# Kernel tuning notes

Hardware: AMD Instinct MI355X
Metric: run time of the kernel (lower is better)

## Reference

```python
import jax, jax.numpy as jnp
import numpy as np

N_NODES = 50000
N_EDGES = 800000
NFEAT = 128
NHID = 128


def gcn_conv(x, edge_index, W, b):
    """PyG GCNConv: add self-loops, symmetric deg^-1/2 normalization, scatter-add."""
    n = x.shape[0]
    loop = jnp.arange(n, dtype=edge_index.dtype)
    row = jnp.concatenate([edge_index[0], loop])  # source nodes
    col = jnp.concatenate([edge_index[1], loop])  # target nodes
    ones = jnp.ones(row.shape[0], dtype=x.dtype)
    deg = jax.ops.segment_sum(ones, col, num_segments=n)
    dinv = jnp.where(deg > 0, jax.lax.rsqrt(deg), 0.0).astype(x.dtype)
    norm = dinv[row] * dinv[col]  # [E+N]
    h = x @ W  # [n, out]
    msg = h[row] * norm[:, None]  # gather + scale, [E+N, out]
    out = jax.ops.segment_sum(msg, col, num_segments=n)  # scatter-add
    return out + b


def setup_inputs() -> dict:
    key = jax.random.key(0)
    kx, ke, k1, k2 = jax.random.split(key, 4)
    x = jax.random.normal(kx, (N_NODES, NFEAT), dtype=jnp.float32)
    edge_index = jax.random.randint(ke, (2, N_EDGES), 0, N_NODES, dtype=jnp.int32)
    s1 = 1.0 / np.sqrt(NFEAT)
    s2 = 1.0 / np.sqrt(NHID)
    W1 = jax.random.uniform(k1, (NFEAT, NHID), jnp.float32, -s1, s1)
    b1 = jnp.zeros((NHID,), jnp.float32)
    W2 = jax.random.uniform(k2, (NHID, NHID), jnp.float32, -s2, s2)
    b2 = jnp.zeros((NHID,), jnp.float32)
    return {"x": x, "edge_index": edge_index, "W1": W1, "b1": b1, "W2": W2, "b2": b2}


def reference(x, edge_index, W1, b1, W2, b2):
    # DGI.forward -> encoder z: relu(GCNConv) x2, dropout=0, no layernorm
    h = jax.nn.relu(gcn_conv(x, edge_index, W1, b1))
    z = jax.nn.relu(gcn_conv(h, edge_index, W2, b2))
    return z
```

## Files before the change

### kernel.cpp

```cpp
#include <hip/hip_runtime.h>
#include <hip/hip_fp16.h>


#define NBK 98
#define BSH 9
#define BCAP 10240

typedef _Float16 f16x8 __attribute__((ext_vector_type(8)));
typedef float f32x4 __attribute__((ext_vector_type(4)));

__global__ __launch_bounds__(256) void k_bucket(const int* __restrict__ row,
                                                const int* __restrict__ col,
                                                int* __restrict__ bcur,
                                                unsigned int* __restrict__ arena,
                                                int E) {
  __shared__ int hist[NBK];
  __shared__ int basec[NBK];
  int tid = threadIdx.x;
  if (tid < NBK) hist[tid] = 0;
  __syncthreads();
  int base = blockIdx.x * 2048;
  int cc[8], rr[8], bb[8];
#pragma unroll
  for (int j = 0; j < 8; ++j) {
    int e = base + j * 256 + tid;
    bb[j] = -1;
    if (e < E) {
      cc[j] = col[e];
      rr[j] = row[e];
      bb[j] = cc[j] >> BSH;
      atomicAdd(&hist[bb[j]], 1);
    }
  }
  __syncthreads();
  if (tid < NBK && hist[tid] > 0)
    basec[tid] = atomicAdd(&bcur[tid], hist[tid]);
  __syncthreads();
#pragma unroll
  for (int j = 0; j < 8; ++j) {
    if (bb[j] >= 0) {
      int pos = atomicAdd(&basec[bb[j]], 1);
      if (pos < BCAP)
        arena[(size_t)bb[j] * BCAP + pos] =
            ((unsigned int)rr[j] << BSH) | (unsigned int)(cc[j] & 511);
    }
  }
}

__global__ __launch_bounds__(256) void k_csr(const int* __restrict__ bcur,
                                             const unsigned int* __restrict__ arena,
                                             int* __restrict__ offs,
                                             float* __restrict__ dinv,
                                             int* __restrict__ esrc, int n) {
  __shared__ int hist[512];
  __shared__ int psum[256];
  int b = blockIdx.x, tid = threadIdx.x;
  hist[tid] = 0;
  hist[tid + 256] = 0;
  __syncthreads();
  int m = min(bcur[b], BCAP);
  const unsigned int* a = arena + (size_t)b * BCAP;
  for (int i = tid; i < m; i += 256) atomicAdd(&hist[a[i] & 511], 1);
  __syncthreads();

  psum[tid] = (tid < b && tid < NBK) ? min(bcur[tid], BCAP) : 0;
  __syncthreads();
#pragma unroll
  for (int d = 128; d > 0; d >>= 1) {
    if (tid < d) psum[tid] += psum[tid + d];
    __syncthreads();
  }
  int base = psum[0];
  __syncthreads();

  int a0 = hist[2 * tid], a1 = hist[2 * tid + 1];
  int pair = a0 + a1;
  psum[tid] = pair;
  __syncthreads();
#pragma unroll
  for (int d = 1; d < 256; d <<= 1) {
    int add = (tid >= d) ? psum[tid - d] : 0;
    __syncthreads();
    psum[tid] += add;
    __syncthreads();
  }
  int excl = psum[tid] - pair;
  int o0 = base + excl, o1 = o0 + a0;

  int nb0 = b << BSH;
  int node0 = nb0 + 2 * tid, node1 = node0 + 1;
  if (node0 < n) {
    offs[node0] = o0;
    dinv[node0] = rsqrtf((float)(a0 + 1));
  }
  if (node1 < n) {
    offs[node1] = o1;
    dinv[node1] = rsqrtf((float)(a1 + 1));
  }
  if (b == NBK - 1 && tid == 255) offs[n] = base + psum[255];
  __syncthreads();

  hist[2 * tid] = o0;
  hist[2 * tid + 1] = o1;
  __syncthreads();
  for (int i = tid; i < m; i += 256) {
    unsigned int p = a[i];
    int pos = atomicAdd(&hist[p & 511], 1);
    esrc[pos] = (int)(p >> BSH);
  }
}

__global__ __launch_bounds__(256) void k_prepW(const float* __restrict__ W1,
                                               const float* __restrict__ W2,
                                               __half* __restrict__ Wt1,
                                               __half* __restrict__ Wt2,
                                               int* __restrict__ bcur) {
  int i = blockIdx.x * 256 + threadIdx.x;
  int n = i >> 7, k = i & 127;
  Wt1[i] = (__half)W1[k * 128 + n];
  Wt2[i] = (__half)W2[k * 128 + n];
  if (i < NBK) bcur[i] = 0;
}

__device__ inline uint4 loadA16(const float* A, int grow, int k16, int M) {
  if (grow >= M) return make_uint4(0, 0, 0, 0);
  const float4* p = (const float4*)(A + (size_t)grow * 128 + k16 * 8);
  float4 f0 = p[0], f1 = p[1];
  __half2 h0 = __floats2half2_rn(f0.x, f0.y);
  __half2 h1 = __floats2half2_rn(f0.z, f0.w);
  __half2 h2 = __floats2half2_rn(f1.x, f1.y);
  __half2 h3 = __floats2half2_rn(f1.z, f1.w);
  uint4 u;
  u.x = *(unsigned int*)&h0;
  u.y = *(unsigned int*)&h1;
  u.z = *(unsigned int*)&h2;
  u.w = *(unsigned int*)&h3;
  return u;
}
__device__ inline uint4 loadA16(const __half* A, int grow, int k16, int M) {
  if (grow >= M) return make_uint4(0, 0, 0, 0);
  return *(const uint4*)(A + (size_t)grow * 128 + k16 * 8);
}

template <typename AT>
__global__ __launch_bounds__(256) void k_gemm(const AT* __restrict__ A,
                                              const __half* __restrict__ Wt,
                                              const float* __restrict__ dinv,
                                              __half* __restrict__ C, int M) {
  __shared__ char smem[16384 + 32768];
  char* Al = smem;
  char* Bl = smem + 16384;
  int tid = threadIdx.x;
  int row0 = blockIdx.x * 64;

  const uint4* Wt4 = (const uint4*)Wt;
#pragma unroll
  for (int i = 0; i < 8; ++i) {
    int c = tid + 256 * i;
    int n = c >> 4, k16 = c & 15;
    uint4 v = Wt4[c];
    *(uint4*)(Bl + n * 256 + ((k16 * 16) ^ ((n & 7) << 4))) = v;
  }
#pragma unroll
  for (int i = 0; i < 4; ++i) {
    int c = tid + 256 * i;
    int r = c >> 4, k16 = c & 15;
    uint4 v = loadA16(A, row0 + r, k16, M);
    *(uint4*)(Al + r * 256 + ((k16 * 16) ^ ((r & 7) << 4))) = v;
  }
  __syncthreads();

  int w = tid >> 6, l = tid & 63;
  int lr = l & 15, lq = l >> 4;
  f32x4 acc[8] = {};
#pragma unroll
  for (int kc = 0; kc < 4; ++kc) {
    int c16 = kc * 4 + lq;
    int ar = w * 16 + lr;
    f16x8 av = *(const f16x8*)(Al + ar * 256 + ((c16 * 16) ^ ((lr & 7) << 4)));
#pragma unroll
    for (int nt = 0; nt < 8; ++nt) {
      int n = nt * 16 + lr;
      f16x8 bv = *(const f16x8*)(Bl + n * 256 + ((c16 * 16) ^ ((n & 7) << 4)));
      acc[nt] = __builtin_amdgcn_mfma_f32_16x16x32_f16(av, bv, acc[nt], 0, 0, 0);
    }
  }

  int orow = row0 + w * 16 + lq * 4;
#pragma unroll
  for (int r = 0; r < 4; ++r) {
    int grow = orow + r;
    if (grow < M) {
      float dv = dinv[grow];
#pragma unroll
      for (int nt = 0; nt < 8; ++nt)
        C[(size_t)grow * 128 + nt * 16 + lr] = (__half)(acc[nt][r] * dv);
    }
  }
}

template <bool FP16OUT>
__global__ __launch_bounds__(256) void k_agg(const __half* __restrict__ hs,
                                             const int* __restrict__ offs,
                                             const int* __restrict__ esrc,
                                             const float* __restrict__ dinv,
                                             const float* __restrict__ bias,
                                             void* __restrict__ outp, int n) {
  int gw = (blockIdx.x * 256 + threadIdx.x) >> 6;
  int lane = threadIdx.x & 63;
  if (gw >= n) return;
  float di = dinv[gw];
  const unsigned int* base = (const unsigned int*)hs;
  unsigned int su = base[(size_t)gw * 64 + lane];
  float2 v = __half22float2(*(__half2*)&su);
  float ax = v.x, ay = v.y;
  int e0 = offs[gw], e1 = offs[gw + 1];
  int e = e0;
  for (; e + 16 <= e1; e += 16) {
    int s[16];
#pragma unroll
    for (int j = 0; j < 16; ++j) s[j] = esrc[e + j];
    unsigned int u[16];
#pragma unroll
    for (int j = 0; j < 16; ++j) u[j] = base[(size_t)s[j] * 64 + lane];
#pragma unroll
    for (int j = 0; j < 16; ++j) {
      float2 hv = __half22float2(*(__half2*)&u[j]);
      ax += hv.x;
      ay += hv.y;
    }
  }
  for (; e + 4 <= e1; e += 4) {
    int s[4];
#pragma unroll
    for (int j = 0; j < 4; ++j) s[j] = esrc[e + j];
    unsigned int u[4];
#pragma unroll
    for (int j = 0; j < 4; ++j) u[j] = base[(size_t)s[j] * 64 + lane];
#pragma unroll
    for (int j = 0; j < 4; ++j) {
      float2 hv = __half22float2(*(__half2*)&u[j]);
      ax += hv.x;
      ay += hv.y;
    }
  }
  for (; e < e1; ++e) {
    unsigned int u = base[(size_t)esrc[e] * 64 + lane];
    float2 hv = __half22float2(*(__half2*)&u);
    ax += hv.x;
    ay += hv.y;
  }
  float2 bv = ((const float2*)bias)[lane];
  float ox = fmaxf(fmaf(ax, di, bv.x), 0.f);
  float oy = fmaxf(fmaf(ay, di, bv.y), 0.f);
  if (FP16OUT) {
    __half2 p = __floats2half2_rn(ox, oy);
    ((unsigned int*)outp)[(size_t)gw * 64 + lane] = *(unsigned int*)&p;
  } else {
    ((float2*)outp)[(size_t)gw * 64 + lane] = make_float2(ox, oy);
  }
}

extern "C" void kernel_launch(void* const* d_in, const int* in_sizes, int n_in,
                              void* d_out, int out_size, void* d_ws, size_t ws_size,
                              hipStream_t stream) {
  const float* x  = (const float*)d_in[0];
  const int*   ei = (const int*)d_in[1];
  const float* W1 = (const float*)d_in[2];
  const float* b1 = (const float*)d_in[3];
  const float* W2 = (const float*)d_in[4];
  const float* b2 = (const float*)d_in[5];
  const int n = in_sizes[0] / 128;
  const int E = in_sizes[1] / 2;
  const int* row = ei;
  const int* col = ei + E;

  char* ws = (char*)d_ws;
  size_t off = 0;
  auto alloc = [&](size_t bytes) -> void* {
    void* p = ws + off;
    off = (off + bytes + 255) & ~(size_t)255;
    return p;
  };
  int*          offs  = (int*)alloc((size_t)(n + 1) * 4);
  float*        dinv  = (float*)alloc((size_t)n * 4);
  int*          bcur  = (int*)alloc(NBK * 4);
  int*          esrc  = (int*)alloc((size_t)E * 4);
  unsigned int* arena = (unsigned int*)alloc((size_t)NBK * BCAP * 4);
  __half*       Wt1   = (__half*)alloc(128 * 128 * 2);
  __half*       Wt2   = (__half*)alloc(128 * 128 * 2);
  __half*       h_tmp = (__half*)alloc((size_t)n * 128 * 2);
  __half*       h16   = (__half*)alloc((size_t)n * 128 * 2);
  (void)ws_size; (void)n_in; (void)out_size;

  k_prepW<<<64, 256, 0, stream>>>(W1, W2, Wt1, Wt2, bcur);
  k_bucket<<<(E + 2047) / 2048, 256, 0, stream>>>(row, col, bcur, arena, E);
  k_csr<<<NBK, 256, 0, stream>>>(bcur, arena, offs, dinv, esrc, n);

  const int gb = (n + 63) / 64;
  const int ab = (n * 64 + 255) / 256;
  k_gemm<float><<<gb, 256, 0, stream>>>(x, Wt1, dinv, h_tmp, n);
  k_agg<true><<<ab, 256, 0, stream>>>(h_tmp, offs, esrc, dinv, b1, h16, n);
  k_gemm<__half><<<gb, 256, 0, stream>>>(h16, Wt2, dinv, h_tmp, n);
  k_agg<false><<<ab, 256, 0, stream>>>(h_tmp, offs, esrc, dinv, b2, d_out, n);
}
```

Measured before the change: 139.7 us.

## Fuse layer-1 aggregation with layer-2 GEMM and merge weight prep into bucketing

Layer-1 aggregation now writes its relu'd fp16 rows straight into shared memory, and the same block runs the second-layer MFMA GEMM on them. This removes the h16 intermediate round trip through global memory and one kernel launch. Weight transposition is folded into the bucketing kernel as extra blocks, and the bucket counter reset becomes a memset. The cost is lower parallelism in the fused kernel: each wave aggregates 16 nodes one after another instead of one node per wave across many blocks, so latency hiding for the gathers may drop.

Measured after the change: 181.7 us. 1.3x slower.

```diff
diff --git a/kernel.cpp b/kernel.cpp
--- a/kernel.cpp
+++ b/kernel.cpp
@@ -5,18 +5,26 @@
 #define NBK 98
 #define BSH 9
 #define BCAP 10240
+#define NBB 391
 
 typedef _Float16 f16x8 __attribute__((ext_vector_type(8)));
 typedef float f32x4 __attribute__((ext_vector_type(4)));
 
-__global__ __launch_bounds__(256) void k_bucket(const int* __restrict__ row,
-                                                const int* __restrict__ col,
-                                                int* __restrict__ bcur,
-                                                unsigned int* __restrict__ arena,
-                                                int E) {
+__global__ __launch_bounds__(256) void k_prep_bucket(
+    const int* __restrict__ row, const int* __restrict__ col,
+    int* __restrict__ bcur, unsigned int* __restrict__ arena, int E,
+    const float* __restrict__ W1, const float* __restrict__ W2,
+    __half* __restrict__ Wt1, __half* __restrict__ Wt2) {
+  int tid = threadIdx.x;
+  if (blockIdx.x >= NBB) {
+    int i = (blockIdx.x - NBB) * 256 + tid;
+    int n = i >> 7, k = i & 127;
+    Wt1[i] = (__half)W1[k * 128 + n];
+    Wt2[i] = (__half)W2[k * 128 + n];
+    return;
+  }
   __shared__ int hist[NBK];
   __shared__ int basec[NBK];
-  int tid = threadIdx.x;
   if (tid < NBK) hist[tid] = 0;
   __syncthreads();
   int base = blockIdx.x * 2048;
@@ -108,18 +116,6 @@
     int pos = atomicAdd(&hist[p & 511], 1);
     esrc[pos] = (int)(p >> BSH);
   }
-}
-
-__global__ __launch_bounds__(256) void k_prepW(const float* __restrict__ W1,
-                                               const float* __restrict__ W2,
-                                               __half* __restrict__ Wt1,
-                                               __half* __restrict__ Wt2,
-                                               int* __restrict__ bcur) {
-  int i = blockIdx.x * 256 + threadIdx.x;
-  int n = i >> 7, k = i & 127;
-  Wt1[i] = (__half)W1[k * 128 + n];
-  Wt2[i] = (__half)W2[k * 128 + n];
-  if (i < NBK) bcur[i] = 0;
 }
 
 __device__ inline uint4 loadA16(const float* A, int grow, int k16, int M) {
@@ -137,13 +133,8 @@
   u.w = *(unsigned int*)&h3;
   return u;
 }
-__device__ inline uint4 loadA16(const __half* A, int grow, int k16, int M) {
-  if (grow >= M) return make_uint4(0, 0, 0, 0);
-  return *(const uint4*)(A + (size_t)grow * 128 + k16 * 8);
-}
-
-template <typename AT>
-__global__ __launch_bounds__(256) void k_gemm(const AT* __restrict__ A,
+
+__global__ __launch_bounds__(256) void k_gemm(const float* __restrict__ A,
                                               const __half* __restrict__ Wt,
                                               const float* __restrict__ dinv,
                                               __half* __restrict__ C, int M) {
@@ -158,8 +149,7 @@
   for (int i = 0; i < 8; ++i) {
     int c = tid + 256 * i;
     int n = c >> 4, k16 = c & 15;
-    uint4 v = Wt4[c];
-    *(uint4*)(Bl + n * 256 + ((k16 * 16) ^ ((n & 7) << 4))) = v;
+    *(uint4*)(Bl + n * 256 + ((k16 * 16) ^ ((n & 7) << 4))) = Wt4[c];
   }
 #pragma unroll
   for (int i = 0; i < 4; ++i) {
@@ -199,13 +189,117 @@
   }
 }
 
-template <bool FP16OUT>
+__global__ __launch_bounds__(256) void k_aggemm(
+    const __half* __restrict__ hs1, const int* __restrict__ offs,
+    const int* __restrict__ esrc, const float* __restrict__ dinv,
+    const float* __restrict__ b1, const __half* __restrict__ Wt2,
+    __half* __restrict__ hs2, int M) {
+  __shared__ char smem[16384 + 32768];
+  char* Al = smem;
+  char* Bl = smem + 16384;
+  int tid = threadIdx.x;
+  int row0 = blockIdx.x * 64;
+
+  const uint4* Wt4 = (const uint4*)Wt2;
+#pragma unroll
+  for (int i = 0; i < 8; ++i) {
+    int c = tid + 256 * i;
+    int n = c >> 4, k16 = c & 15;
+    *(uint4*)(Bl + n * 256 + ((k16 * 16) ^ ((n & 7) << 4))) = Wt4[c];
+  }
+
+  int w = tid >> 6, l = tid & 63;
+  const unsigned int* base = (const unsigned int*)hs1;
+  float2 bv = ((const float2*)b1)[l];
+  for (int i = 0; i < 16; ++i) {
+    int g = row0 + w * 16 + i;
+    unsigned int outu = 0;
+    if (g < M) {
+      float di = dinv[g];
+      unsigned int su = base[(size_t)g * 64 + l];
+      float2 v = __half22float2(*(__half2*)&su);
+      float ax = v.x, ay = v.y;
+      int e0 = offs[g], e1 = offs[g + 1];
+      int e = e0;
+      for (; e + 16 <= e1; e += 16) {
+        int s[16];
+#pragma unroll
+        for (int j = 0; j < 16; ++j) s[j] = esrc[e + j];
+        unsigned int u[16];
+#pragma unroll
+        for (int j = 0; j < 16; ++j) u[j] = base[(size_t)s[j] * 64 + l];
+#pragma unroll
+        for (int j = 0; j < 16; ++j) {
+          float2 hv = __half22float2(*(__half2*)&u[j]);
+          ax += hv.x;
+          ay += hv.y;
+        }
+      }
+      for (; e + 4 <= e1; e += 4) {
+        int s[4];
+#pragma unroll
+        for (int j = 0; j < 4; ++j) s[j] = esrc[e + j];
+        unsigned int u[4];
+#pragma unroll
+        for (int j = 0; j < 4; ++j) u[j] = base[(size_t)s[j] * 64 + l];
+#pragma unroll
+        for (int j = 0; j < 4; ++j) {
+          float2 hv = __half22float2(*(__half2*)&u[j]);
+          ax += hv.x;
+          ay += hv.y;
+        }
+      }
+      for (; e < e1; ++e) {
+        unsigned int u = base[(size_t)esrc[e] * 64 + l];
+        float2 hv = __half22float2(*(__half2*)&u);
+        ax += hv.x;
+        ay += hv.y;
+      }
+      float ox = fmaxf(fmaf(ax, di, bv.x), 0.f);
+      float oy = fmaxf(fmaf(ay, di, bv.y), 0.f);
+      __half2 p = __floats2half2_rn(ox, oy);
+      outu = *(unsigned int*)&p;
+    }
+    int r = w * 16 + i;
+    *(unsigned int*)(Al + r * 256 + (((l >> 2) * 16) ^ ((r & 7) << 4)) +
+                     (l & 3) * 4) = outu;
+  }
+  __syncthreads();
+
+  int lr = l & 15, lq = l >> 4;
+  f32x4 acc[8] = {};
+#pragma unroll
+  for (int kc = 0; kc < 4; ++kc) {
+    int c16 = kc * 4 + lq;
+    int ar = w * 16 + lr;
+    f16x8 av = *(const f16x8*)(Al + ar * 256 + ((c16 * 16) ^ ((lr & 7) << 4)));
+#pragma unroll
+    for (int nt = 0; nt < 8; ++nt) {
+      int n = nt * 16 + lr;
+      f16x8 bvv = *(const f16x8*)(Bl + n * 256 + ((c16 * 16) ^ ((n & 7) << 4)));
+      acc[nt] = __builtin_amdgcn_mfma_f32_16x16x32_f16(av, bvv, acc[nt], 0, 0, 0);
+    }
+  }
+
+  int orow = row0 + w * 16 + lq * 4;
+#pragma unroll
+  for (int r = 0; r < 4; ++r) {
+    int grow = orow + r;
+    if (grow < M) {
+      float dv = dinv[grow];
+#pragma unroll
+      for (int nt = 0; nt < 8; ++nt)
+        hs2[(size_t)grow * 128 + nt * 16 + lr] = (__half)(acc[nt][r] * dv);
+    }
+  }
+}
+
 __global__ __launch_bounds__(256) void k_agg(const __half* __restrict__ hs,
                                              const int* __restrict__ offs,
                                              const int* __restrict__ esrc,
                                              const float* __restrict__ dinv,
                                              const float* __restrict__ bias,
-                                             void* __restrict__ outp, int n) {
+                                             float* __restrict__ out, int n) {
   int gw = (blockIdx.x * 256 + threadIdx.x) >> 6;
   int lane = threadIdx.x & 63;
   if (gw >= n) return;
@@ -253,12 +347,7 @@
   float2 bv = ((const float2*)bias)[lane];
   float ox = fmaxf(fmaf(ax, di, bv.x), 0.f);
   float oy = fmaxf(fmaf(ay, di, bv.y), 0.f);
-  if (FP16OUT) {
-    __half2 p = __floats2half2_rn(ox, oy);
-    ((unsigned int*)outp)[(size_t)gw * 64 + lane] = *(unsigned int*)&p;
-  } else {
-    ((float2*)outp)[(size_t)gw * 64 + lane] = make_float2(ox, oy);
-  }
+  ((float2*)(out + (size_t)gw * 128))[lane] = make_float2(ox, oy);
 }
 
 extern "C" void kernel_launch(void* const* d_in, const int* in_sizes, int n_in,
@@ -289,18 +378,18 @@
   unsigned int* arena = (unsigned int*)alloc((size_t)NBK * BCAP * 4);
   __half*       Wt1   = (__half*)alloc(128 * 128 * 2);
   __half*       Wt2   = (__half*)alloc(128 * 128 * 2);
-  __half*       h_tmp = (__half*)alloc((size_t)n * 128 * 2);
-  __half*       h16   = (__half*)alloc((size_t)n * 128 * 2);
+  __half*       hs1   = (__half*)alloc((size_t)n * 128 * 2);
+  __half*       hs2   = (__half*)alloc((size_t)n * 128 * 2);
   (void)ws_size; (void)n_in; (void)out_size;
 
-  k_prepW<<<64, 256, 0, stream>>>(W1, W2, Wt1, Wt2, bcur);
-  k_bucket<<<(E + 2047) / 2048, 256, 0, stream>>>(row, col, bcur, arena, E);
+  hipMemsetAsync(bcur, 0, NBK * 4, stream);
+  k_prep_bucket<<<NBB + 64, 256, 0, stream>>>(row, col, bcur, arena, E,
+                                              W1, W2, Wt1, Wt2);
   k_csr<<<NBK, 256, 0, stream>>>(bcur, arena, offs, dinv, esrc, n);
 
   const int gb = (n + 63) / 64;
   const int ab = (n * 64 + 255) / 256;
-  k_gemm<float><<<gb, 256, 0, stream>>>(x, Wt1, dinv, h_tmp, n);
-  k_agg<true><<<ab, 256, 0, stream>>>(h_tmp, offs, esrc, dinv, b1, h16, n);
-  k_gemm<__half><<<gb, 256, 0, stream>>>(h16, Wt2, dinv, h_tmp, n);
-  k_agg<false><<<ab, 256, 0, stream>>>(h_tmp, offs, esrc, dinv, b2, d_out, n);
-}
+  k_gemm<<<gb, 256, 0, stream>>>(x, Wt1, dinv, hs1, n);
+  k_aggemm<<<gb, 256, 0, stream>>>(hs1, offs, esrc, dinv, b1, Wt2, hs2, n);
+  k_agg<<<ab, 256, 0, stream>>>(hs2, offs, esrc, dinv, b2, (float*)d_out, n);
+}
```
